# Kernel optimization log

Measured on AMD Instinct MI355X. Metric: run time of the kernel, lower is better.

The kernel has to match this reference:

```python
import jax, jax.numpy as jnp
import numpy as np
from jax import lax


def _conv(x, w, b):
    # x: (B,C,H,W), w: (O,I,3,3) -> SAME padding, stride 1 (NCHW/OIHW)
    y = lax.conv_general_dilated(x, w, (1, 1), 'SAME',
                                 dimension_numbers=('NCHW', 'OIHW', 'NCHW'))
    return y + b[None, :, None, None]


def _maxpool2(x):
    return lax.reduce_window(x, -jnp.inf, lax.max, (1, 1, 2, 2), (1, 1, 2, 2), 'VALID')


def setup_inputs() -> dict:
    key = jax.random.key(0)
    ks = jax.random.split(key, 16)
    B, C, H, W = 4096, 3, 32, 32
    E, NC = 4, 10
    s = 0.05
    x = jax.random.normal(ks[0], (B, C, H, W), jnp.float32)
    return {
        'x': x,
        # gating network
        'gw_conv': jax.random.normal(ks[1], (16, C, 3, 3), jnp.float32) * s,
        'gb_conv': jnp.zeros((16,), jnp.float32),
        'gw_fc': jax.random.normal(ks[2], (E, 16), jnp.float32) * s,
        'gb_fc': jnp.zeros((E,), jnp.float32),
        # experts (stacked over leading expert dim E)
        'ew_conv1': jax.random.normal(ks[3], (E, 32, C, 3, 3), jnp.float32) * s,
        'eb_conv1': jnp.zeros((E, 32), jnp.float32),
        'ew_conv2': jax.random.normal(ks[4], (E, 64, 32, 3, 3), jnp.float32) * s,
        'eb_conv2': jnp.zeros((E, 64), jnp.float32),
        'ew_fc1': jax.random.normal(ks[5], (E, 128, 64 * 8 * 8), jnp.float32) * s,
        'eb_fc1': jnp.zeros((E, 128), jnp.float32),
        'ew_fc2': jax.random.normal(ks[6], (E, NC, 128), jnp.float32) * s,
        'eb_fc2': jnp.zeros((E, NC), jnp.float32),
    }


def reference(x, gw_conv, gb_conv, gw_fc, gb_fc,
              ew_conv1, eb_conv1, ew_conv2, eb_conv2,
              ew_fc1, eb_fc1, ew_fc2, eb_fc2):
    B = x.shape[0]
    E = gw_fc.shape[0]
    NC = ew_fc2.shape[1]
    TOP_K = 1

    # ---- Router: conv -> relu -> global avg pool -> linear -> softmax ----
    h = jax.nn.relu(_conv(x, gw_conv, gb_conv))          # (B,16,32,32)
    pooled = h.mean(axis=(2, 3))                          # (B,16)
    router_probs = jax.nn.softmax(pooled @ gw_fc.T + gb_fc, axis=1)  # (B,E)

    # ---- Top-k hard routing -> dense per-expert combine weights ----
    topk_probs, topk_idx = lax.top_k(router_probs, TOP_K)  # (B,k)
    weights = jnp.zeros((B, E), x.dtype).at[
        jnp.arange(B)[:, None], topk_idx].add(topk_probs)  # (B,E), zero off-topk

    # ---- Experts: run each expert densely, weight, accumulate ----
    # (expert_out * 0 == 0 exactly, so this matches torch's gather/scatter-add)
    final = jnp.zeros((B, NC), x.dtype)
    for i in range(E):  # small fixed expert count
        h1 = _maxpool2(jax.nn.relu(_conv(x, ew_conv1[i], eb_conv1[i])))   # (B,32,16,16)
        h2 = _maxpool2(jax.nn.relu(_conv(h1, ew_conv2[i], eb_conv2[i])))  # (B,64,8,8)
        f = h2.reshape(B, -1)                                             # (B,4096)
        f = jax.nn.relu(f @ ew_fc1[i].T + eb_fc1[i])                      # (B,128)
        out = f @ ew_fc2[i].T + eb_fc2[i]                                 # (B,NC)
        final = final + out * weights[:, i:i + 1]

    # ---- Load-balancing auxiliary loss (MSE vs uniform) ----
    mean_probs = router_probs.mean(axis=0)
    aux_loss = jnp.mean((mean_probs - 1.0 / E) ** 2)
    return final, router_probs, aux_loss
```

## Files before the change

### kernel.cpp

```cpp
#include <hip/hip_runtime.h>
#include <hip/hip_bf16.h>
#include <cstdint>
#include <cstddef>

#define B_N 4096
typedef short short8 __attribute__((ext_vector_type(8)));
typedef float f32x4 __attribute__((ext_vector_type(4)));
typedef float f32x2 __attribute__((ext_vector_type(2)));

static constexpr size_t H2B_OFF    = 0;
static constexpr size_t POOLED_OFF = 8388608;
static constexpr size_t EIDX_OFF   = POOLED_OFF + (size_t)B_N * 16;
static constexpr size_t EW_OFF     = EIDX_OFF + B_N;
static constexpr size_t ORDER_OFF  = EW_OFF + B_N;
static constexpr size_t CNT_OFF    = ORDER_OFF + (size_t)4 * B_N;
static constexpr size_t PSUM_OFF   = CNT_OFF + 4;
static constexpr size_t W2R_OFF    = PSUM_OFF + 4;
static constexpr size_t W1R_OFF    = W2R_OFF + 36864;
static constexpr size_t W1C_OFF    = W1R_OFF + 1048576;

__device__ __forceinline__ unsigned int f2bf(float f) {
  unsigned int u = __float_as_uint(f);
  return (u + 0x7fffu + ((u >> 16) & 1u)) >> 16;
}
__device__ __forceinline__ unsigned int pkbf(float lo, float hi) {
  float2 f; f.x = lo; f.y = hi;
  __hip_bfloat162 b = __float22bfloat162_rn(f);
  union { __hip_bfloat162 b; unsigned u; } c; c.b = b; return c.u;
}

__global__ __launch_bounds__(256) void k_front(
    const float* __restrict__ wfc1, unsigned short* __restrict__ w1r,
    const float* __restrict__ wc2, unsigned short* __restrict__ w2r,
    const float* __restrict__ wc1, unsigned short* __restrict__ w1c,
    int* __restrict__ counts) {
  const int rb = blockIdx.x, t = threadIdx.x;
  if (rb < 2048) {
    const int i = rb * 256 + t;
    const float4 v = ((const float4*)wfc1)[i];
    ushort4 u;
    u.x = (unsigned short)f2bf(v.x); u.y = (unsigned short)f2bf(v.y);
    u.z = (unsigned short)f2bf(v.z); u.w = (unsigned short)f2bf(v.w);
    *(ushort4*)(w1r + 4 * (size_t)i) = u;
  } else if (rb < 2336) {
    if (rb == 2048 && t < 8) counts[t] = 0;
    const int i = (rb - 2048) * 256 + t;
    if (i < 4 * 9 * 64 * 32) {
      const int ic = i & 31, j = i >> 5;
      const int oc = j & 63, j2 = j >> 6;
      const int s = j2 % 9, e = j2 / 9;
      w2r[i] = (unsigned short)f2bf(wc2[(((size_t)e * 64 + oc) * 32 + ic) * 9 + s]);
    }
  } else {
    const int i = (rb - 2336) * 256 + t;
    if (i < 4096) {
      const int j = i & 7, n16 = (i >> 3) & 15, q = (i >> 7) & 3, nt = (i >> 9) & 1, e = i >> 10;
      const int k = q * 8 + j;
      float v = 0.f;
      if (k < 27) {
        const int ky = k / 9, c = k % 9, kx = c / 3, ic = c % 3;
        v = wc1[((e * 32 + nt * 16 + n16) * 3 + ic) * 9 + ky * 3 + kx];
      }
      w1c[i] = (unsigned short)f2bf(v);
    }
  }
}

__device__ __forceinline__ short8 gather_a(const float* __restrict__ base,
                                           const int* goff, bool isq1, bool isq3) {
  const float a0 = base[goff[0]];
  float       a1 = base[goff[0] + 1];
  const float b0 = base[goff[1]], b1 = base[goff[1] + 1];
  const float c0 = base[goff[2]], c1 = base[goff[2] + 1];
  const float d0 = base[goff[3]], d1 = base[goff[3] + 1];
  a1 = isq1 ? base[102] : a1;
  union { unsigned u[4]; short8 s; } r;
  r.u[0] = pkbf(a0, a1);
  r.u[1] = pkbf(b0, isq3 ? 0.f : b1);
  r.u[2] = isq3 ? 0u : pkbf(c0, c1);
  r.u[3] = isq3 ? 0u : pkbf(d0, d1);
  return r.s;
}

__global__ __launch_bounds__(256, 3) void k_experts_conv(const float* __restrict__ x,
    const float* __restrict__ gw, const float* __restrict__ gb,
    const float* __restrict__ gwfc, const float* __restrict__ gbfc,
    const unsigned short* __restrict__ w1c, const float* __restrict__ b1g,
    const unsigned short* __restrict__ w2r, const float* __restrict__ b2g,
    unsigned short* __restrict__ h2b, float* __restrict__ probs_out,
    float* __restrict__ ewt, int* __restrict__ counts, int* __restrict__ order) {
  __shared__ __align__(16) float xpi[3572];
  __shared__ __align__(16) unsigned short h1s[18 * 18 * 36];
  __shared__ float red[16 * 33];
  __shared__ float pooled_s[16];
  __shared__ int es;
  const int b = blockIdx.x, t = threadIdx.x;
  {
    uint4 z4 = make_uint4(0, 0, 0, 0);
    uint4* z1 = (uint4*)h1s;
    for (int i = t; i < 1458; i += 256) z1[i] = z4;
    uint4* z2 = (uint4*)xpi;
    for (int i = t; i < 893; i += 256) z2[i] = z4;
  }
  __syncthreads();
  const float4* x4 = (const float4*)(x + (size_t)b * 3072);
  for (int i = t; i < 768; i += 256) {
    float4 v = x4[i];
    int flat = i * 4, ic = flat >> 10, rem = flat & 1023, row = rem >> 5, col = rem & 31;
    float* d = &xpi[(row + 1) * 102 + (col + 1) * 3 + ic];
    d[0] = v.x; d[3] = v.y; d[6] = v.z; d[9] = v.w;
  }
  __syncthreads();
  {
    const int ty = t >> 4, tx = t & 15;
    f32x2 wp[3][4][3];
#pragma unroll
    for (int ic = 0; ic < 3; ++ic)
#pragma unroll
    for (int rr = 0; rr < 4; ++rr) {
      const float* p = &xpi[(2 * ty + rr) * 102 + (2 * tx) * 3 + ic];
      const float r0 = p[0], r1 = p[3], r2 = p[6], r3 = p[9];
      wp[ic][rr][0] = (f32x2){r0, r1};
      wp[ic][rr][1] = (f32x2){r1, r2};
      wp[ic][rr][2] = (f32x2){r2, r3};
    }
    float sums[16];
#pragma unroll
    for (int oc = 0; oc < 16; ++oc) {
      const float bias = gb[oc];
      f32x2 A0 = {bias, bias};
      f32x2 A1 = {bias, bias};
#pragma unroll
      for (int ic = 0; ic < 3; ++ic)
#pragma unroll
      for (int ky = 0; ky < 3; ++ky)
#pragma unroll
      for (int kx = 0; kx < 3; ++kx) {
        const float wv2 = gw[oc * 27 + ic * 9 + ky * 3 + kx];
        const f32x2 ws = {wv2, wv2};
        A0 = __builtin_elementwise_fma(wp[ic][ky][kx], ws, A0);
        A1 = __builtin_elementwise_fma(wp[ic][ky + 1][kx], ws, A1);
      }
      sums[oc] = fmaxf(A0.x, 0.f) + fmaxf(A0.y, 0.f) + fmaxf(A1.x, 0.f) + fmaxf(A1.y, 0.f);
    }
    const int rl = t & 63, wid = t >> 6;
#pragma unroll
    for (int oc = 0; oc < 16; ++oc) {
      float s = sums[oc];
      s += __shfl_xor(s, 1);
      s += __shfl_xor(s, 2);
      s += __shfl_xor(s, 4);
      sums[oc] = s;
    }
    if ((rl & 7) == 0) {
      const int slot = wid * 8 + (rl >> 3);
#pragma unroll
      for (int oc = 0; oc < 16; ++oc) red[oc * 33 + slot] = sums[oc];
    }
    __syncthreads();
    if (t < 16) {
      float s = 0.f;
#pragma unroll
      for (int i = 0; i < 32; ++i) s += red[t * 33 + i];
      pooled_s[t] = s * (1.f / 1024.f);
    }
    __syncthreads();
    if (t == 0) {
      float l[4];
#pragma unroll
      for (int j = 0; j < 4; ++j) {
        float s = gbfc[j];
#pragma unroll
        for (int i = 0; i < 16; ++i) s += pooled_s[i] * gwfc[j * 16 + i];
        l[j] = s;
      }
      const float mx = fmaxf(fmaxf(l[0], l[1]), fmaxf(l[2], l[3]));
      float ex[4], ssum = 0.f;
#pragma unroll
      for (int j = 0; j < 4; ++j) { ex[j] = expf(l[j] - mx); ssum += ex[j]; }
      const float inv = 1.f / ssum;
      float p[4];
#pragma unroll
      for (int j = 0; j < 4; ++j) p[j] = ex[j] * inv;
      *(float4*)(probs_out + (size_t)b * 4) = make_float4(p[0], p[1], p[2], p[3]);
      int em = 0; float pm = p[0];
#pragma unroll
      for (int j = 1; j < 4; ++j) if (p[j] > pm) { pm = p[j]; em = j; }
      ewt[b] = pm;
      const int slot = atomicAdd(&counts[em], 1);
      order[em * B_N + slot] = b;
      es = em;
    }
    __syncthreads();
  }
  const int e = __builtin_amdgcn_readfirstlane(es);
  const int lane = t & 63, wv = t >> 6;
  const int n16 = lane & 15, q = lane >> 4;
  {
    const bool isq1 = (q == 1), isq3 = (q == 3);
    const short8 wb0 = *(const short8*)(w1c + (((e * 2 + 0) * 4 + q) * 16 + n16) * 8);
    const short8 wb1 = *(const short8*)(w1c + (((e * 2 + 1) * 4 + q) * 16 + n16) * 8);
    const float bias0 = b1g[e * 32 + n16];
    const float bias1 = b1g[e * 32 + 16 + n16];
    int goff[4];
#pragma unroll
    for (int t4 = 0; t4 < 4; ++t4) {
      const int p0 = q * 8 + 2 * t4;
      const int r = (p0 * 939) >> 13;
      goff[t4] = r * 102 + (p0 - 9 * r);
    }
    for (int pid = 0; pid < 8; ++pid) {
      const int pairid = wv * 8 + pid;
      const int yp = pairid >> 1, xh = pairid & 1;
      const float* baseA = &xpi[(2 * yp) * 102 + (xh * 16 + n16) * 3];
      const short8 afA = gather_a(baseA, goff, isq1, isq3);
      const short8 afB = gather_a(baseA + 102, goff, isq1, isq3);
      f32x4 aA0 = {bias0, bias0, bias0, bias0}, aA1 = {bias1, bias1, bias1, bias1};
      f32x4 aB0 = aA0, aB1 = aA1;
      aA0 = __builtin_amdgcn_mfma_f32_16x16x32_bf16(afA, wb0, aA0, 0, 0, 0);
      aA1 = __builtin_amdgcn_mfma_f32_16x16x32_bf16(afA, wb1, aA1, 0, 0, 0);
      aB0 = __builtin_amdgcn_mfma_f32_16x16x32_bf16(afB, wb0, aB0, 0, 0, 0);
      aB1 = __builtin_amdgcn_mfma_f32_16x16x32_bf16(afB, wb1, aB1, 0, 0, 0);
      const int px = xh * 8 + 2 * q;
      unsigned short* hw = &h1s[((yp + 1) * 18 + (px + 1)) * 36];
      const float p00 = fmaxf(fmaxf(fmaxf(aA0[0], aA0[1]), fmaxf(aB0[0], aB0[1])), 0.f);
      const float p01 = fmaxf(fmaxf(fmaxf(aA0[2], aA0[3]), fmaxf(aB0[2], aB0[3])), 0.f);
      const float p10 = fmaxf(fmaxf(fmaxf(aA1[0], aA1[1]), fmaxf(aB1[0], aB1[1])), 0.f);
      const float p11 = fmaxf(fmaxf(fmaxf(aA1[2], aA1[3]), fmaxf(aB1[2], aB1[3])), 0.f);
      hw[n16]           = (unsigned short)f2bf(p00);
      hw[16 + n16]      = (unsigned short)f2bf(p10);
      hw[36 + n16]      = (unsigned short)f2bf(p01);
      hw[36 + 16 + n16] = (unsigned short)f2bf(p11);
    }
  }
  __syncthreads();
  {
    const unsigned short* wbase = w2r + (size_t)e * 18432 + n16 * 32 + q * 8;
    float bz[4];
#pragma unroll
    for (int nt = 0; nt < 4; ++nt) bz[nt] = b2g[e * 64 + nt * 16 + n16];
    f32x4 acc[4][4];
#pragma unroll
    for (int mt4 = 0; mt4 < 4; ++mt4)
#pragma unroll
      for (int nt = 0; nt < 4; ++nt) {
        acc[mt4][nt][0] = bz[nt]; acc[mt4][nt][1] = bz[nt];
        acc[mt4][nt][2] = bz[nt]; acc[mt4][nt][3] = bz[nt];
      }
    short8 Bc[4];
#pragma unroll
    for (int nt = 0; nt < 4; ++nt) Bc[nt] = *(const short8*)(wbase + nt * 512);
#pragma unroll
    for (int s = 0; s < 9; ++s) {
      const int ky = s / 3, kx = s % 3;
      short8 Bn[4];
      if (s < 8) {
#pragma unroll
        for (int nt = 0; nt < 4; ++nt)
          Bn[nt] = *(const short8*)(wbase + (s + 1) * 2048 + nt * 512);
      }
#pragma unroll
      for (int mt4 = 0; mt4 < 4; ++mt4) {
        const int mt = wv * 4 + mt4;
        const short8 af = *(const short8*)&h1s[((mt + ky) * 18 + n16 + kx) * 36 + q * 8];
#pragma unroll
        for (int nt = 0; nt < 4; ++nt)
          acc[mt4][nt] = __builtin_amdgcn_mfma_f32_16x16x32_bf16(af, Bc[nt], acc[mt4][nt], 0, 0, 0);
      }
      if (s < 8) {
#pragma unroll
        for (int nt = 0; nt < 4; ++nt) Bc[nt] = Bn[nt];
      }
    }
    __syncthreads();
    float* h2s = (float*)h1s;
#pragma unroll
    for (int u2 = 0; u2 < 2; ++u2) {
      const int py = wv * 2 + u2;
#pragma unroll
      for (int nt = 0; nt < 4; ++nt) {
        const f32x4 a = acc[2 * u2][nt], c = acc[2 * u2 + 1][nt];
        float2 pv;
        pv.x = fmaxf(fmaxf(fmaxf(a[0], a[1]), fmaxf(c[0], c[1])), 0.f);
        pv.y = fmaxf(fmaxf(fmaxf(a[2], a[3]), fmaxf(c[2], c[3])), 0.f);
        *(float2*)&h2s[(nt * 16 + n16) * 68 + py * 8 + 2 * q] = pv;
      }
    }
  }
  __syncthreads();
  {
    const float* h2s = (const float*)h1s;
    unsigned short* dst = h2b + (size_t)b * 4096;
#pragma unroll
    for (int j = 0; j < 2; ++j) {
      const int f = 8 * (t + 256 * j);
      const float* src = &h2s[(f >> 6) * 68 + (f & 63)];
      float4 v0 = *(const float4*)src;
      float4 v1 = *(const float4*)(src + 4);
      unsigned int p0 = pkbf(v0.x, v0.y);
      unsigned int p1 = pkbf(v0.z, v0.w);
      unsigned int p2 = pkbf(v1.x, v1.y);
      unsigned int p3 = pkbf(v1.z, v1.w);
      *(uint4*)(dst + f) = make_uint4(p0, p1, p2, p3);
    }
  }
}

__global__ __launch_bounds__(256) void k_fc(const unsigned short* __restrict__ h2b,
    const unsigned short* __restrict__ w1r, const float* __restrict__ b1g,
    const float* __restrict__ w2g, const float* __restrict__ b2g,
    const int* __restrict__ counts, const int* __restrict__ order,
    const float* __restrict__ ew, float* __restrict__ outp) {
  const int bid = blockIdx.x;
  const int t = threadIdx.x;
  if (bid == 0) {
    const float* pr = outp + 40960;
    float s0 = 0.f, s1 = 0.f, s2 = 0.f, s3 = 0.f;
    for (int i = t; i < 4096; i += 256) {
      const float4 v = *(const float4*)(pr + (size_t)i * 4);
      s0 += v.x; s1 += v.y; s2 += v.z; s3 += v.w;
    }
#pragma unroll
    for (int k = 1; k < 64; k <<= 1) {
      s0 += __shfl_xor(s0, k); s1 += __shfl_xor(s1, k);
      s2 += __shfl_xor(s2, k); s3 += __shfl_xor(s3, k);
    }
    __shared__ float ax[4][4];
    if ((t & 63) == 0) {
      const int w = t >> 6;
      ax[w][0] = s0; ax[w][1] = s1; ax[w][2] = s2; ax[w][3] = s3;
    }
    __syncthreads();
    if (t == 0) {
      float a = 0.f;
#pragma unroll
      for (int j = 0; j < 4; ++j) {
        const float mp = (ax[0][j] + ax[1][j] + ax[2][j] + ax[3][j]) * (1.f / 4096.f) - 0.25f;
        a += mp * mp;
      }
      outp[57344] = a * 0.25f;
    }
  }
  const int e = bid >> 8, tile = bid & 255;
  const int n = counts[e];
  const int base = tile * 16;
  if (base >= n) return;
  __shared__ int sb[16];
  __shared__ float wgt[16];
  __shared__ __align__(16) unsigned short As[16][280];
  __shared__ float f1s[16 * 132];
  if (t < 16) {
    const int idx = base + t;
    const int s = order[e * B_N + ((idx < n) ? idx : base)];
    sb[t] = s; wgt[t] = ew[s];
  }
  __syncthreads();
  const int lane = t & 63, wv = t >> 6;
  const int n16 = lane & 15, q = lane >> 4;
  const int oc0 = wv * 32 + n16;
  const int oc1 = wv * 32 + 16 + n16;
  const unsigned short* wb0 = w1r + ((size_t)(e * 128 + oc0)) * 4096 + q * 8;
  const unsigned short* wb1 = w1r + ((size_t)(e * 128 + oc1)) * 4096 + q * 8;
  f32x4 acc0 = {0.f, 0.f, 0.f, 0.f}, acc1 = {0.f, 0.f, 0.f, 0.f};
  const int ldrow = t >> 4, ldseg = t & 15;
  const unsigned short* asrc = h2b + (size_t)sb[ldrow] * 4096;
  uint4 r0 = *(const uint4*)(asrc + ldseg * 8);
  uint4 r1 = *(const uint4*)(asrc + (ldseg + 16) * 8);
  for (int kc = 0; kc < 4096; kc += 256) {
    *(uint4*)&As[ldrow][ldseg * 8] = r0;
    *(uint4*)&As[ldrow][(ldseg + 16) * 8] = r1;
    __syncthreads();
    if (kc + 256 < 4096) {
      r0 = *(const uint4*)(asrc + (kc + 256) + ldseg * 8);
      r1 = *(const uint4*)(asrc + (kc + 256) + (ldseg + 16) * 8);
    }
#pragma unroll
    for (int ks = 0; ks < 8; ++ks) {
      const short8 af = *(const short8*)&As[n16][ks * 32 + q * 8];
      const short8 bf0 = *(const short8*)(wb0 + kc + ks * 32);
      const short8 bf1 = *(const short8*)(wb1 + kc + ks * 32);
      acc0 = __builtin_amdgcn_mfma_f32_16x16x32_bf16(af, bf0, acc0, 0, 0, 0);
      acc1 = __builtin_amdgcn_mfma_f32_16x16x32_bf16(af, bf1, acc1, 0, 0, 0);
    }
    __syncthreads();
  }
  const float* b1 = b1g + e * 128;
  const float bb0 = b1[oc0], bb1 = b1[oc1];
#pragma unroll
  for (int r = 0; r < 4; ++r) {
    const int m = q * 4 + r;
    f1s[m * 132 + oc0] = fmaxf(acc0[r] + bb0, 0.f);
    f1s[m * 132 + oc1] = fmaxf(acc1[r] + bb1, 0.f);
  }
  __syncthreads();
  int m = n - base; if (m > 16) m = 16;
  if (t < 160) {
    const int r = t / 10, o = t - r * 10;
    if (r < m) {
      const float* w2 = w2g + (e * 10 + o) * 128;
      float s = b2g[e * 10 + o];
#pragma unroll 8
      for (int c = 0; c < 128; ++c) s += f1s[r * 132 + c] * w2[c];
      outp[(size_t)sb[r] * 10 + o] = s * wgt[r];
    }
  }
}

extern "C" void kernel_launch(void* const* d_in, const int* in_sizes, int n_in,
                              void* d_out, int out_size, void* d_ws, size_t ws_size,
                              hipStream_t stream) {
  const float* x        = (const float*)d_in[0];
  const float* gw_conv  = (const float*)d_in[1];
  const float* gb_conv  = (const float*)d_in[2];
  const float* gw_fc    = (const float*)d_in[3];
  const float* gb_fc    = (const float*)d_in[4];
  const float* ew_conv1 = (const float*)d_in[5];
  const float* eb_conv1 = (const float*)d_in[6];
  const float* ew_conv2 = (const float*)d_in[7];
  const float* eb_conv2 = (const float*)d_in[8];
  const float* ew_fc1   = (const float*)d_in[9];
  const float* eb_fc1   = (const float*)d_in[10];
  const float* ew_fc2   = (const float*)d_in[11];
  const float* eb_fc2   = (const float*)d_in[12];
  float* out = (float*)d_out;
  float* ws  = (float*)d_ws;

  unsigned short* h2b = (unsigned short*)(ws + H2B_OFF);
  float* ew     = ws + EW_OFF;
  int*   order  = (int*)(ws + ORDER_OFF);
  int*   counts = (int*)(ws + CNT_OFF);
  unsigned short* w2r = (unsigned short*)(ws + W2R_OFF);
  unsigned short* w1r = (unsigned short*)(ws + W1R_OFF);
  unsigned short* w1c = (unsigned short*)(ws + W1C_OFF);

  k_front<<<2352, 256, 0, stream>>>(ew_fc1, w1r, ew_conv2, w2r, ew_conv1, w1c, counts);
  k_experts_conv<<<4096, 256, 0, stream>>>(x, gw_conv, gb_conv, gw_fc, gb_fc,
                                           w1c, eb_conv1, w2r, eb_conv2, h2b,
                                           out + 40960, ew, counts, order);
  k_fc<<<1024, 256, 0, stream>>>(h2b, w1r, eb_fc1, ew_fc2, eb_fc2,
                                 counts, order, ew, out);
}
```

Measured before the change: 246.8 us.

## Fuse weight-conversion prologue into conv kernel via ticket work queue and gate

Removes the separate weight-conversion kernel. Its jobs (conv2, conv1 and fc1 bf16 repacking) are now pulled by conv blocks from a global atomic ticket counter before they start their own work. Blocks spin on a completion gate counter only right before they need the conv weights, and the counters are zeroed with a memset. This saves one kernel launch and the gap between kernels, and lets the fc1 conversion overlap the conv work. In exchange it adds atomics, a spin-wait, and a dependence on forward progress of the resident blocks.

```diff
diff --git a/kernel.cpp b/kernel.cpp
--- a/kernel.cpp
+++ b/kernel.cpp
@@ -27,43 +27,6 @@
   float2 f; f.x = lo; f.y = hi;
   __hip_bfloat162 b = __float22bfloat162_rn(f);
   union { __hip_bfloat162 b; unsigned u; } c; c.b = b; return c.u;
-}
-
-__global__ __launch_bounds__(256) void k_front(
-    const float* __restrict__ wfc1, unsigned short* __restrict__ w1r,
-    const float* __restrict__ wc2, unsigned short* __restrict__ w2r,
-    const float* __restrict__ wc1, unsigned short* __restrict__ w1c,
-    int* __restrict__ counts) {
-  const int rb = blockIdx.x, t = threadIdx.x;
-  if (rb < 2048) {
-    const int i = rb * 256 + t;
-    const float4 v = ((const float4*)wfc1)[i];
-    ushort4 u;
-    u.x = (unsigned short)f2bf(v.x); u.y = (unsigned short)f2bf(v.y);
-    u.z = (unsigned short)f2bf(v.z); u.w = (unsigned short)f2bf(v.w);
-    *(ushort4*)(w1r + 4 * (size_t)i) = u;
-  } else if (rb < 2336) {
-    if (rb == 2048 && t < 8) counts[t] = 0;
-    const int i = (rb - 2048) * 256 + t;
-    if (i < 4 * 9 * 64 * 32) {
-      const int ic = i & 31, j = i >> 5;
-      const int oc = j & 63, j2 = j >> 6;
-      const int s = j2 % 9, e = j2 / 9;
-      w2r[i] = (unsigned short)f2bf(wc2[(((size_t)e * 64 + oc) * 32 + ic) * 9 + s]);
-    }
-  } else {
-    const int i = (rb - 2336) * 256 + t;
-    if (i < 4096) {
-      const int j = i & 7, n16 = (i >> 3) & 15, q = (i >> 7) & 3, nt = (i >> 9) & 1, e = i >> 10;
-      const int k = q * 8 + j;
-      float v = 0.f;
-      if (k < 27) {
-        const int ky = k / 9, c = k % 9, kx = c / 3, ic = c % 3;
-        v = wc1[((e * 32 + nt * 16 + n16) * 3 + ic) * 9 + ky * 3 + kx];
-      }
-      w1c[i] = (unsigned short)f2bf(v);
-    }
-  }
 }
 
 __device__ __forceinline__ short8 gather_a(const float* __restrict__ base,
@@ -85,8 +48,11 @@
 __global__ __launch_bounds__(256, 3) void k_experts_conv(const float* __restrict__ x,
     const float* __restrict__ gw, const float* __restrict__ gb,
     const float* __restrict__ gwfc, const float* __restrict__ gbfc,
-    const unsigned short* __restrict__ w1c, const float* __restrict__ b1g,
-    const unsigned short* __restrict__ w2r, const float* __restrict__ b2g,
+    const float* __restrict__ wc1, const float* __restrict__ b1g,
+    const float* __restrict__ wc2, const float* __restrict__ b2g,
+    const float* __restrict__ wfc1,
+    unsigned short* __restrict__ w1c, unsigned short* __restrict__ w2r,
+    unsigned short* __restrict__ w1r,
     unsigned short* __restrict__ h2b, float* __restrict__ probs_out,
     float* __restrict__ ewt, int* __restrict__ counts, int* __restrict__ order) {
   __shared__ __align__(16) float xpi[3572];
@@ -94,7 +60,42 @@
   __shared__ float red[16 * 33];
   __shared__ float pooled_s[16];
   __shared__ int es;
+  __shared__ int jslot;
   const int b = blockIdx.x, t = threadIdx.x;
+  int* const ticket = counts + 4;
+  int* const gate   = counts + 5;
+  for (;;) {
+    if (t == 0) jslot = atomicAdd(ticket, 1);
+    __syncthreads();
+    const int j = jslot;
+    if (j >= 2352) break;
+    if (j < 288) {
+      const int i = j * 256 + t;
+      const int ic = i & 31, jj = i >> 5;
+      const int oc = jj & 63, j2 = jj >> 6;
+      const int s = j2 % 9, e = j2 / 9;
+      w2r[i] = (unsigned short)f2bf(wc2[(((size_t)e * 64 + oc) * 32 + ic) * 9 + s]);
+    } else if (j < 304) {
+      const int i = (j - 288) * 256 + t;
+      const int jx = i & 7, n16r = (i >> 3) & 15, qr = (i >> 7) & 3, nt = (i >> 9) & 1, e = i >> 10;
+      const int k = qr * 8 + jx;
+      float v = 0.f;
+      if (k < 27) {
+        const int ky = k / 9, c = k % 9, kx = c / 3, ic = c % 3;
+        v = wc1[((e * 32 + nt * 16 + n16r) * 3 + ic) * 9 + ky * 3 + kx];
+      }
+      w1c[i] = (unsigned short)f2bf(v);
+    } else {
+      const int i = (j - 304) * 256 + t;
+      const float4 v = ((const float4*)wfc1)[i];
+      ushort4 u;
+      u.x = (unsigned short)f2bf(v.x); u.y = (unsigned short)f2bf(v.y);
+      u.z = (unsigned short)f2bf(v.z); u.w = (unsigned short)f2bf(v.w);
+      *(ushort4*)(w1r + 4 * (size_t)i) = u;
+    }
+    __syncthreads();
+    if (t == 0 && j < 304) { __threadfence(); atomicAdd(gate, 1); }
+  }
   {
     uint4 z4 = make_uint4(0, 0, 0, 0);
     uint4* z1 = (uint4*)h1s;
@@ -193,6 +194,11 @@
     }
     __syncthreads();
   }
+  if (t == 0) {
+    while (atomicAdd(gate, 0) < 304) __builtin_amdgcn_s_sleep(2);
+    __threadfence();
+  }
+  __syncthreads();
   const int e = __builtin_amdgcn_readfirstlane(es);
   const int lane = t & 63, wv = t >> 6;
   const int n16 = lane & 15, q = lane >> 4;
@@ -433,9 +439,10 @@
   unsigned short* w1r = (unsigned short*)(ws + W1R_OFF);
   unsigned short* w1c = (unsigned short*)(ws + W1C_OFF);
 
-  k_front<<<2352, 256, 0, stream>>>(ew_fc1, w1r, ew_conv2, w2r, ew_conv1, w1c, counts);
+  hipMemsetAsync((void*)counts, 0, 24, stream);
   k_experts_conv<<<4096, 256, 0, stream>>>(x, gw_conv, gb_conv, gw_fc, gb_fc,
-                                           w1c, eb_conv1, w2r, eb_conv2, h2b,
+                                           ew_conv1, eb_conv1, ew_conv2, eb_conv2,
+                                           ew_fc1, w1c, w2r, w1r, h2b,
                                            out + 40960, ew, counts, order);
   k_fc<<<1024, 256, 0, stream>>>(h2b, w1r, eb_fc1, ew_fc2, eb_fc2,
                                  counts, order, ew, out);
```

Result: slower. 443.7 us (+79.8%).
